# Kernel optimization log

Hardware: AMD Instinct MI355X
Metric: run time of the kernel (lower is better)

## Reference

```python
import jax, jax.numpy as jnp
import numpy as np

DYN = 16  # number of dynamic input features; x rows are [dynamic || static]


def setup_inputs() -> dict:
    key = jax.random.key(0)
    ks = jax.random.split(key, 20)
    T, S, H, O = 16384, 32, 512, 1
    sc_h = 1.0 / np.sqrt(H)
    inp = {
        "x": jax.random.normal(ks[0], (T, DYN + S), jnp.float32),
        "h0": jax.random.normal(ks[1], (H,), jnp.float32),
        "c0": jax.random.normal(ks[2], (H,), jnp.float32),
        "Wi": jax.random.normal(ks[3], (H, S), jnp.float32) / np.sqrt(S),
        "bi": jax.random.normal(ks[4], (H,), jnp.float32) * 0.1,
        "Wf1": jax.random.normal(ks[5], (H, DYN), jnp.float32) / np.sqrt(DYN),
        "bf1": jax.random.normal(ks[6], (H,), jnp.float32) * 0.1,
        "Wf2": jax.random.normal(ks[7], (H, H), jnp.float32) * sc_h,
        "bf2": jax.random.normal(ks[8], (H,), jnp.float32) * 0.1,
        "Wg1": jax.random.normal(ks[9], (H, DYN), jnp.float32) / np.sqrt(DYN),
        "bg1": jax.random.normal(ks[10], (H,), jnp.float32) * 0.1,
        "Wg2": jax.random.normal(ks[11], (H, H), jnp.float32) * sc_h,
        "bg2": jax.random.normal(ks[12], (H,), jnp.float32) * 0.1,
        "Wo1": jax.random.normal(ks[13], (H, DYN), jnp.float32) / np.sqrt(DYN),
        "bo1": jax.random.normal(ks[14], (H,), jnp.float32) * 0.1,
        "Wo2": jax.random.normal(ks[15], (H, H), jnp.float32) * sc_h,
        "bo2": jax.random.normal(ks[16], (H,), jnp.float32) * 0.1,
        "Wl": jax.random.normal(ks[17], (O, H), jnp.float32) * sc_h,
        "bl": jax.random.normal(ks[18], (O,), jnp.float32) * 0.1,
    }
    return inp


def reference(x, h0, c0, Wi, bi, Wf1, bf1, Wf2, bf2, Wg1, bg1, Wg2, bg2,
              Wo1, bo1, Wo2, bo2, Wl, bl):
    x_dyn = x[:, :DYN]   # [T, DYN]
    x_stat = x[:, DYN:]  # [T, S]
    # input gate depends only on static features -> vectorize over T
    i_all = jax.nn.sigmoid(x_stat @ Wi.T + bi)           # [T, H]
    # precompute dynamic-input projections (both linear biases folded in)
    pf = x_dyn @ Wf1.T + (bf1 + bf2)                      # [T, H]
    pg = x_dyn @ Wg1.T + (bg1 + bg2)
    po = x_dyn @ Wo1.T + (bo1 + bo2)

    def step(carry, ins):
        h, c = carry
        it, xf, xg, xo = ins
        f = jax.nn.sigmoid(xf + h @ Wf2.T)
        g = jnp.tanh(xg + h @ Wg2.T)
        o = jax.nn.sigmoid(xo + h @ Wo2.T)
        c = f * c + it * g
        h = o * jnp.tanh(c)
        return (h, c), h

    (_, _), h_all = jax.lax.scan(step, (h0, c0), (i_all, pf, pg, po))
    out = h_all @ Wl.T + bl                               # [T, O]
    return out
```

## Files before the change

kernel.cpp:

```cpp
#include <hip/hip_runtime.h>

#define T_STEPS 16384
#define HID     512
#define NSLOT   32
#define JPW     16
#define RING_D  8
#define RING_W  1024
#define NPART   (NSLOT * 4)
#define NBLK    256
#define FAST_TRIES 3

typedef unsigned u32x4 __attribute__((ext_vector_type(4)));

__device__ __forceinline__ unsigned ld_agent(const unsigned* p) {
  return __hip_atomic_load(p, __ATOMIC_RELAXED, __HIP_MEMORY_SCOPE_AGENT);
}
__device__ __forceinline__ float sigf(float x) {
  return __fdividef(1.f, 1.f + __expf(-x));
}
__device__ __forceinline__ float tanhfast(float x) {
  x = fminf(fmaxf(x, -15.f), 15.f);
  float e = __expf(2.f * x);
  return 1.f - __fdividef(2.f, e + 1.f);
}

__global__ void init_kernel(float* __restrict__ out,
                            unsigned* __restrict__ ring_fast,
                            unsigned* __restrict__ ring_slow,
                            const float* __restrict__ h0,
                            const float* __restrict__ bl) {
  int i = blockIdx.x * blockDim.x + threadIdx.x;
  if (i < T_STEPS) out[i] = bl[0];
  if (i < RING_D * RING_W) {
    unsigned v = 0;
    int slot = i >> 10;
    int w = i & (RING_W - 1);
    if (slot == RING_D - 1) {
      unsigned bits = __float_as_uint(h0[w >> 1]);
      v = (w & 1) ? ((bits << 16) | 1u) : ((bits & 0xFFFF0000u) | 1u);
    }
    ring_fast[i] = v;
    ring_slow[i] = v;
  }
}

__global__ void finalize_kernel(const float* __restrict__ part,
                                const float* __restrict__ bl,
                                float* __restrict__ out) {
  int t = blockIdx.x * blockDim.x + threadIdx.x;
  float s = bl[0];
#pragma unroll 8
  for (int i = 0; i < NPART; ++i) s += part[i * T_STEPS + t];
  out[t] = s;
}

__global__ __launch_bounds__(256, 1) void lstm_scan(
    const float* __restrict__ x,  const float* __restrict__ c0,
    const float* __restrict__ Wi, const float* __restrict__ bi,
    const float* __restrict__ Wf1,const float* __restrict__ bf1,
    const float* __restrict__ Wf2,const float* __restrict__ bf2,
    const float* __restrict__ Wg1,const float* __restrict__ bg1,
    const float* __restrict__ Wg2,const float* __restrict__ bg2,
    const float* __restrict__ Wo1,const float* __restrict__ bo1,
    const float* __restrict__ Wo2,const float* __restrict__ bo2,
    const float* __restrict__ Wl, float* __restrict__ out,
    unsigned* __restrict__ ring_fast, unsigned* __restrict__ ring_slow,
    float* __restrict__ part)
{
  if ((blockIdx.x & 7) != 0) return;
  const int slot = blockIdx.x >> 3;

  const int tid = threadIdx.x;
  const int jl  = tid >> 4;
  const int s   = tid & 15;
  const int jg  = slot * JPW + jl;

  __shared__ __align__(16) float hbuf[2][16 * 36];
  __shared__ float4 xbuf[2][12];

  float4 wf[8], wg[8], wo[8];
  {
    const float4* pf = (const float4*)(Wf2 + jg * HID + s * 32);
    const float4* pg = (const float4*)(Wg2 + jg * HID + s * 32);
    const float4* po = (const float4*)(Wo2 + jg * HID + s * 32);
#pragma unroll
    for (int r = 0; r < 8; ++r) { wf[r] = pf[r]; wg[r] = pg[r]; wo[r] = po[r]; }
  }
  float4 wx[8];
  float xb = 0.f;
#pragma unroll
  for (int r = 0; r < 8; ++r) wx[r] = make_float4(0.f, 0.f, 0.f, 0.f);
  if (s == 0) {
    const float4* p = (const float4*)(Wi + jg * 32);
#pragma unroll
    for (int r = 0; r < 8; ++r) wx[r] = p[r];
    xb = bi[jg];
  } else if (s == 1) {
    const float4* p = (const float4*)(Wf1 + jg * 16);
#pragma unroll
    for (int r = 0; r < 4; ++r) wx[r] = p[r];
    xb = bf1[jg] + bf2[jg];
  } else if (s == 2) {
    const float4* p = (const float4*)(Wg1 + jg * 16);
#pragma unroll
    for (int r = 0; r < 4; ++r) wx[r] = p[r];
    xb = bg1[jg] + bg2[jg];
  } else if (s == 3) {
    const float4* p = (const float4*)(Wo1 + jg * 16);
#pragma unroll
    for (int r = 0; r < 4; ++r) wx[r] = p[r];
    xb = bo1[jg] + bo2[jg];
  }

  float cst = c0[jg];
  const float wl = Wl[jg];

  float4 xpre = make_float4(0.f, 0.f, 0.f, 0.f);
  if (tid < 12) {
    xbuf[0][tid] = *(const float4*)(x + 4 * tid);
    xpre = *(const float4*)(x + 48 + 4 * tid);
  }
  __syncthreads();

  for (int t = 0; t < T_STEPS; ++t) {
    if (tid < 12) {
      xbuf[(t + 1) & 1][tid] = xpre;
      int tn = (t + 2 < T_STEPS) ? t + 2 : T_STEPS - 1;
      xpre = *(const float4*)(x + tn * 48 + 4 * tid);
    }
    float pr = xb;
    if (s < 4) {
      const float4* xv = &xbuf[t & 1][(s == 0) ? 4 : 0];
#pragma unroll
      for (int r = 0; r < 4; ++r) {
        float4 vv = xv[r], w = wx[r];
        pr = fmaf(w.x, vv.x, pr); pr = fmaf(w.y, vv.y, pr);
        pr = fmaf(w.z, vv.z, pr); pr = fmaf(w.w, vv.w, pr);
      }
      if (s == 0) {
#pragma unroll
        for (int r = 4; r < 8; ++r) {
          float4 vv = xv[r], w = wx[r];
          pr = fmaf(w.x, vv.x, pr); pr = fmaf(w.y, vv.y, pr);
          pr = fmaf(w.z, vv.z, pr); pr = fmaf(w.w, vv.w, pr);
        }
      }
    }
    float accf = (s == 1) ? pr : 0.f;
    float accg = (s == 2) ? pr : 0.f;
    float acco = (s == 3) ? pr : 0.f;
    const float ipre = pr;

    const unsigned want = (unsigned)(t + 1);
    const unsigned ring_off =
        (((unsigned)(t - 1)) & (RING_D - 1)) * RING_W + 4 * tid;
    unsigned a, b, c2, d2;
    unsigned matched = 0;
    {
      const unsigned* pf = ring_fast + ring_off;
#pragma unroll 1
      for (int k = 0; k < FAST_TRIES; ++k) {
        u32x4 v;
        asm volatile("global_load_dwordx4 %0, %1, off sc0\n\ts_waitcnt vmcnt(0)"
                     : "=v"(v) : "v"(pf) : "memory");
        a = v[0]; b = v[1]; c2 = v[2]; d2 = v[3];
        if (!(((a ^ want) | (b ^ want) | (c2 ^ want) | (d2 ^ want)) & 0xFFFFu)) {
          matched = 1;
          break;
        }
      }
    }
    if (!matched) {
      const unsigned* pw = ring_slow + ring_off;
      do {
        a = ld_agent(pw); b = ld_agent(pw + 1);
        c2 = ld_agent(pw + 2); d2 = ld_agent(pw + 3);
      } while (((a ^ want) | (b ^ want) | (c2 ^ want) | (d2 ^ want)) & 0xFFFFu);
    }
    unsigned bits0 = (a  & 0xFFFF0000u) | (b  >> 16);
    unsigned bits1 = (c2 & 0xFFFF0000u) | (d2 >> 16);
    {
      int idx = 2 * tid + 4 * (tid >> 4);
      *(float2*)(&hbuf[t & 1][idx]) =
          make_float2(__uint_as_float(bits0), __uint_as_float(bits1));
    }
    __syncthreads();

    const float* hb = &hbuf[t & 1][s * 36];
#pragma unroll
    for (int r = 0; r < 8; ++r) {
      float4 hv = *(const float4*)(hb + 4 * r);
      accf = fmaf(wf[r].x, hv.x, accf); accf = fmaf(wf[r].y, hv.y, accf);
      accf = fmaf(wf[r].z, hv.z, accf); accf = fmaf(wf[r].w, hv.w, accf);
      accg = fmaf(wg[r].x, hv.x, accg); accg = fmaf(wg[r].y, hv.y, accg);
      accg = fmaf(wg[r].z, hv.z, accg); accg = fmaf(wg[r].w, hv.w, accg);
      acco = fmaf(wo[r].x, hv.x, acco); acco = fmaf(wo[r].y, hv.y, acco);
      acco = fmaf(wo[r].z, hv.z, acco); acco = fmaf(wo[r].w, hv.w, acco);
    }
#pragma unroll
    for (int m = 1; m <= 8; m <<= 1) {
      accf += __shfl_xor(accf, m, 16);
      accg += __shfl_xor(accg, m, 16);
      acco += __shfl_xor(acco, m, 16);
    }
    float f  = sigf(accf);
    float g  = tanhfast(accg);
    float o  = sigf(acco);
    float it = sigf(ipre);
    cst = fmaf(f, cst, it * g);
    float hj = o * tanhfast(cst);

    if (s == 0) {
      unsigned bits = __float_as_uint(hj);
      unsigned tag  = (unsigned)(t + 2);
      unsigned long long v64 =
          (unsigned long long)((bits & 0xFFFF0000u) | tag) |
          ((unsigned long long)((bits << 16) | tag) << 32);
      unsigned dst_off = (t & (RING_D - 1)) * RING_W + 2 * jg;
      __hip_atomic_store((unsigned long long*)(ring_fast + dst_off), v64,
                         __ATOMIC_RELAXED, __HIP_MEMORY_SCOPE_WORKGROUP);
      __hip_atomic_store((unsigned long long*)(ring_slow + dst_off), v64,
                         __ATOMIC_RELAXED, __HIP_MEMORY_SCOPE_AGENT);
    }
    float val = (s == 0) ? wl * hj : 0.f;
    val += __shfl_xor(val, 16, 64);
    val += __shfl_xor(val, 32, 64);
    if ((tid & 63) == 0) {
      if (part) {
        part[(slot * 4 + (tid >> 6)) * T_STEPS + t] = val;
      } else {
        atomicAdd(out + t, val);
      }
    }
  }
}

extern "C" void kernel_launch(void* const* d_in, const int* in_sizes, int n_in,
                              void* d_out, int out_size, void* d_ws, size_t ws_size,
                              hipStream_t stream) {
  const float* x   = (const float*)d_in[0];
  const float* h0  = (const float*)d_in[1];
  const float* c0  = (const float*)d_in[2];
  const float* Wi  = (const float*)d_in[3];
  const float* bi  = (const float*)d_in[4];
  const float* Wf1 = (const float*)d_in[5];
  const float* bf1 = (const float*)d_in[6];
  const float* Wf2 = (const float*)d_in[7];
  const float* bf2 = (const float*)d_in[8];
  const float* Wg1 = (const float*)d_in[9];
  const float* bg1 = (const float*)d_in[10];
  const float* Wg2 = (const float*)d_in[11];
  const float* bg2 = (const float*)d_in[12];
  const float* Wo1 = (const float*)d_in[13];
  const float* bo1 = (const float*)d_in[14];
  const float* Wo2 = (const float*)d_in[15];
  const float* bo2 = (const float*)d_in[16];
  const float* Wl  = (const float*)d_in[17];
  const float* bl  = (const float*)d_in[18];
  float* out = (float*)d_out;

  size_t ring_words = (size_t)RING_D * RING_W;
  unsigned* ring_fast = (unsigned*)d_ws;
  unsigned* ring_slow = ring_fast + ring_words;
  size_t base_bytes = 2 * ring_words * 4;
  size_t part_bytes = (size_t)NPART * T_STEPS * 4;
  float* part = (ws_size >= base_bytes + part_bytes)
                    ? (float*)((char*)d_ws + base_bytes)
                    : nullptr;

  hipLaunchKernelGGL(init_kernel, dim3(64), dim3(256), 0, stream,
                     out, ring_fast, ring_slow, h0, bl);
  hipLaunchKernelGGL(lstm_scan, dim3(NBLK), dim3(256), 0, stream,
                     x, c0, Wi, bi, Wf1, bf1, Wf2, bf2, Wg1, bg1, Wg2, bg2,
                     Wo1, bo1, Wo2, bo2, Wl, out, ring_fast, ring_slow, part);
  if (part) {
    hipLaunchKernelGGL(finalize_kernel, dim3(T_STEPS / 256), dim3(256), 0, stream,
                       part, bl, out);
  }
}
```

Measured before the change: 30.98 ms.

## Unroll recurrence by 8, overlap ring poll with input projection, batch x staging

The time loop is unrolled in blocks of 8 steps. The first ring-buffer poll load is issued before the input-projection FMAs and waited on afterwards, so its latency is hidden behind useful work. Input rows are now staged 8 at a time into shared memory, and partial head outputs are written as float4 pairs once per block instead of once per step. The cross-lane shuffle reduction is replaced with DPP row adds, the barrier becomes a raw s_barrier with an explicit lgkmcnt wait, and the number of fast poll retries is raised. The cost is higher register pressure from the unroll and the pacc array.

```diff
diff --git a/kernel.cpp b/kernel.cpp
--- a/kernel.cpp
+++ b/kernel.cpp
@@ -8,7 +8,7 @@
 #define RING_W  1024
 #define NPART   (NSLOT * 4)
 #define NBLK    256
-#define FAST_TRIES 3
+#define FAST_TRIES 8
 
 typedef unsigned u32x4 __attribute__((ext_vector_type(4)));
 
@@ -22,6 +22,18 @@
   x = fminf(fmaxf(x, -15.f), 15.f);
   float e = __expf(2.f * x);
   return 1.f - __fdividef(2.f, e + 1.f);
+}
+template <int CTRL>
+__device__ __forceinline__ float dpp_xadd(float v) {
+  int t = __builtin_amdgcn_update_dpp(0, __float_as_int(v), CTRL, 0xF, 0xF, true);
+  return v + __int_as_float(t);
+}
+__device__ __forceinline__ float row16_reduce(float v) {
+  v = dpp_xadd<0xB1>(v);
+  v = dpp_xadd<0x4E>(v);
+  v = dpp_xadd<0x141>(v);
+  v = dpp_xadd<0x140>(v);
+  return v;
 }
 
 __global__ void init_kernel(float* __restrict__ out,
@@ -76,7 +88,7 @@
   const int jg  = slot * JPW + jl;
 
   __shared__ __align__(16) float hbuf[2][16 * 36];
-  __shared__ float4 xbuf[2][12];
+  __shared__ __align__(16) float4 xstage[2][96];
 
   float4 wf[8], wg[8], wo[8];
   {
@@ -115,121 +127,135 @@
   float cst = c0[jg];
   const float wl = Wl[jg];
 
+  const int xrow = tid / 12, xcol = tid - 12 * xrow;
   float4 xpre = make_float4(0.f, 0.f, 0.f, 0.f);
-  if (tid < 12) {
-    xbuf[0][tid] = *(const float4*)(x + 4 * tid);
-    xpre = *(const float4*)(x + 48 + 4 * tid);
+  if (tid < 96) {
+    xstage[0][tid] = *(const float4*)(x + xrow * 48 + 4 * xcol);
+    xpre = *(const float4*)(x + (8 + xrow) * 48 + 4 * xcol);
   }
   __syncthreads();
 
-  for (int t = 0; t < T_STEPS; ++t) {
-    if (tid < 12) {
-      xbuf[(t + 1) & 1][tid] = xpre;
-      int tn = (t + 2 < T_STEPS) ? t + 2 : T_STEPS - 1;
-      xpre = *(const float4*)(x + tn * 48 + 4 * tid);
-    }
-    float pr = xb;
-    if (s < 4) {
-      const float4* xv = &xbuf[t & 1][(s == 0) ? 4 : 0];
-#pragma unroll
-      for (int r = 0; r < 4; ++r) {
-        float4 vv = xv[r], w = wx[r];
-        pr = fmaf(w.x, vv.x, pr); pr = fmaf(w.y, vv.y, pr);
-        pr = fmaf(w.z, vv.z, pr); pr = fmaf(w.w, vv.w, pr);
-      }
-      if (s == 0) {
-#pragma unroll
-        for (int r = 4; r < 8; ++r) {
+  float pacc[8];
+
+  for (int tb = 0; tb < T_STEPS / 8; ++tb) {
+#pragma unroll
+    for (int u = 0; u < 8; ++u) {
+      const int t = tb * 8 + u;
+      const unsigned want = (unsigned)(t + 1);
+      const unsigned ring_off =
+          (((unsigned)(t - 1)) & (RING_D - 1)) * RING_W + 4 * tid;
+      const unsigned* pf = ring_fast + ring_off;
+      u32x4 v;
+      asm volatile("global_load_dwordx4 %0, %1, off sc0"
+                   : "=v"(v) : "v"(pf) : "memory");
+      float pr = xb;
+      if (s < 4) {
+        const float4* xv = &xstage[tb & 1][u * 12 + ((s == 0) ? 4 : 0)];
+#pragma unroll
+        for (int r = 0; r < 4; ++r) {
           float4 vv = xv[r], w = wx[r];
           pr = fmaf(w.x, vv.x, pr); pr = fmaf(w.y, vv.y, pr);
           pr = fmaf(w.z, vv.z, pr); pr = fmaf(w.w, vv.w, pr);
         }
-      }
+        if (s == 0) {
+#pragma unroll
+          for (int r = 4; r < 8; ++r) {
+            float4 vv = xv[r], w = wx[r];
+            pr = fmaf(w.x, vv.x, pr); pr = fmaf(w.y, vv.y, pr);
+            pr = fmaf(w.z, vv.z, pr); pr = fmaf(w.w, vv.w, pr);
+          }
+        }
+      }
+      float accf = (s == 1) ? pr : 0.f;
+      float accg = (s == 2) ? pr : 0.f;
+      float acco = (s == 3) ? pr : 0.f;
+      const float ipre = pr;
+
+      asm volatile("s_waitcnt vmcnt(0)" ::: "memory");
+      asm volatile("" : "+v"(v));
+      unsigned a = v[0], b = v[1], c2 = v[2], d2 = v[3];
+      if (((a ^ want) | (b ^ want) | (c2 ^ want) | (d2 ^ want)) & 0xFFFFu) {
+        unsigned matched = 0;
+#pragma unroll 1
+        for (int k = 1; k < FAST_TRIES; ++k) {
+          asm volatile("global_load_dwordx4 %0, %1, off sc0\n\ts_waitcnt vmcnt(0)"
+                       : "=v"(v) : "v"(pf) : "memory");
+          a = v[0]; b = v[1]; c2 = v[2]; d2 = v[3];
+          if (!(((a ^ want) | (b ^ want) | (c2 ^ want) | (d2 ^ want)) & 0xFFFFu)) {
+            matched = 1;
+            break;
+          }
+        }
+        if (!matched) {
+          const unsigned* pw = ring_slow + ring_off;
+          do {
+            a = ld_agent(pw); b = ld_agent(pw + 1);
+            c2 = ld_agent(pw + 2); d2 = ld_agent(pw + 3);
+          } while (((a ^ want) | (b ^ want) | (c2 ^ want) | (d2 ^ want)) & 0xFFFFu);
+        }
+      }
+      unsigned bits0 = (a  & 0xFFFF0000u) | (b  >> 16);
+      unsigned bits1 = (c2 & 0xFFFF0000u) | (d2 >> 16);
+      {
+        int idx = 2 * tid + 4 * (tid >> 4);
+        *(float2*)(&hbuf[t & 1][idx]) =
+            make_float2(__uint_as_float(bits0), __uint_as_float(bits1));
+      }
+      if (u == 7 && tid < 96) {
+        xstage[(tb + 1) & 1][tid] = xpre;
+        int row = (tb + 2) * 8 + xrow;
+        if (row >= T_STEPS) row = T_STEPS - 1;
+        xpre = *(const float4*)(x + row * 48 + 4 * xcol);
+      }
+      asm volatile("s_waitcnt lgkmcnt(0)" ::: "memory");
+      __builtin_amdgcn_s_barrier();
+
+      const float* hb = &hbuf[t & 1][s * 36];
+#pragma unroll
+      for (int r = 0; r < 8; ++r) {
+        float4 hv = *(const float4*)(hb + 4 * r);
+        accf = fmaf(wf[r].x, hv.x, accf); accf = fmaf(wf[r].y, hv.y, accf);
+        accf = fmaf(wf[r].z, hv.z, accf); accf = fmaf(wf[r].w, hv.w, accf);
+        accg = fmaf(wg[r].x, hv.x, accg); accg = fmaf(wg[r].y, hv.y, accg);
+        accg = fmaf(wg[r].z, hv.z, accg); accg = fmaf(wg[r].w, hv.w, accg);
+        acco = fmaf(wo[r].x, hv.x, acco); acco = fmaf(wo[r].y, hv.y, acco);
+        acco = fmaf(wo[r].z, hv.z, acco); acco = fmaf(wo[r].w, hv.w, acco);
+      }
+      accf = row16_reduce(accf);
+      accg = row16_reduce(accg);
+      acco = row16_reduce(acco);
+      float f  = sigf(accf);
+      float g  = tanhfast(accg);
+      float o  = sigf(acco);
+      float it = sigf(ipre);
+      cst = fmaf(f, cst, it * g);
+      float hj = o * tanhfast(cst);
+
+      if (s == 0) {
+        unsigned bits = __float_as_uint(hj);
+        unsigned tag  = (unsigned)(t + 2);
+        unsigned long long v64 =
+            (unsigned long long)((bits & 0xFFFF0000u) | tag) |
+            ((unsigned long long)((bits << 16) | tag) << 32);
+        unsigned dst_off = (t & (RING_D - 1)) * RING_W + 2 * jg;
+        __hip_atomic_store((unsigned long long*)(ring_fast + dst_off), v64,
+                           __ATOMIC_RELAXED, __HIP_MEMORY_SCOPE_WORKGROUP);
+        __hip_atomic_store((unsigned long long*)(ring_slow + dst_off), v64,
+                           __ATOMIC_RELAXED, __HIP_MEMORY_SCOPE_AGENT);
+      }
+      float val = (s == 0) ? wl * hj : 0.f;
+      val += __shfl_xor(val, 16, 64);
+      val += __shfl_xor(val, 32, 64);
+      pacc[u] = val;
     }
-    float accf = (s == 1) ? pr : 0.f;
-    float accg = (s == 2) ? pr : 0.f;
-    float acco = (s == 3) ? pr : 0.f;
-    const float ipre = pr;
-
-    const unsigned want = (unsigned)(t + 1);
-    const unsigned ring_off =
-        (((unsigned)(t - 1)) & (RING_D - 1)) * RING_W + 4 * tid;
-    unsigned a, b, c2, d2;
-    unsigned matched = 0;
-    {
-      const unsigned* pf = ring_fast + ring_off;
-#pragma unroll 1
-      for (int k = 0; k < FAST_TRIES; ++k) {
-        u32x4 v;
-        asm volatile("global_load_dwordx4 %0, %1, off sc0\n\ts_waitcnt vmcnt(0)"
-                     : "=v"(v) : "v"(pf) : "memory");
-        a = v[0]; b = v[1]; c2 = v[2]; d2 = v[3];
-        if (!(((a ^ want) | (b ^ want) | (c2 ^ want) | (d2 ^ want)) & 0xFFFFu)) {
-          matched = 1;
-          break;
-        }
-      }
-    }
-    if (!matched) {
-      const unsigned* pw = ring_slow + ring_off;
-      do {
-        a = ld_agent(pw); b = ld_agent(pw + 1);
-        c2 = ld_agent(pw + 2); d2 = ld_agent(pw + 3);
-      } while (((a ^ want) | (b ^ want) | (c2 ^ want) | (d2 ^ want)) & 0xFFFFu);
-    }
-    unsigned bits0 = (a  & 0xFFFF0000u) | (b  >> 16);
-    unsigned bits1 = (c2 & 0xFFFF0000u) | (d2 >> 16);
-    {
-      int idx = 2 * tid + 4 * (tid >> 4);
-      *(float2*)(&hbuf[t & 1][idx]) =
-          make_float2(__uint_as_float(bits0), __uint_as_float(bits1));
-    }
-    __syncthreads();
-
-    const float* hb = &hbuf[t & 1][s * 36];
-#pragma unroll
-    for (int r = 0; r < 8; ++r) {
-      float4 hv = *(const float4*)(hb + 4 * r);
-      accf = fmaf(wf[r].x, hv.x, accf); accf = fmaf(wf[r].y, hv.y, accf);
-      accf = fmaf(wf[r].z, hv.z, accf); accf = fmaf(wf[r].w, hv.w, accf);
-      accg = fmaf(wg[r].x, hv.x, accg); accg = fmaf(wg[r].y, hv.y, accg);
-      accg = fmaf(wg[r].z, hv.z, accg); accg = fmaf(wg[r].w, hv.w, accg);
-      acco = fmaf(wo[r].x, hv.x, acco); acco = fmaf(wo[r].y, hv.y, acco);
-      acco = fmaf(wo[r].z, hv.z, acco); acco = fmaf(wo[r].w, hv.w, acco);
-    }
-#pragma unroll
-    for (int m = 1; m <= 8; m <<= 1) {
-      accf += __shfl_xor(accf, m, 16);
-      accg += __shfl_xor(accg, m, 16);
-      acco += __shfl_xor(acco, m, 16);
-    }
-    float f  = sigf(accf);
-    float g  = tanhfast(accg);
-    float o  = sigf(acco);
-    float it = sigf(ipre);
-    cst = fmaf(f, cst, it * g);
-    float hj = o * tanhfast(cst);
-
-    if (s == 0) {
-      unsigned bits = __float_as_uint(hj);
-      unsigned tag  = (unsigned)(t + 2);
-      unsigned long long v64 =
-          (unsigned long long)((bits & 0xFFFF0000u) | tag) |
-          ((unsigned long long)((bits << 16) | tag) << 32);
-      unsigned dst_off = (t & (RING_D - 1)) * RING_W + 2 * jg;
-      __hip_atomic_store((unsigned long long*)(ring_fast + dst_off), v64,
-                         __ATOMIC_RELAXED, __HIP_MEMORY_SCOPE_WORKGROUP);
-      __hip_atomic_store((unsigned long long*)(ring_slow + dst_off), v64,
-                         __ATOMIC_RELAXED, __HIP_MEMORY_SCOPE_AGENT);
-    }
-    float val = (s == 0) ? wl * hj : 0.f;
-    val += __shfl_xor(val, 16, 64);
-    val += __shfl_xor(val, 32, 64);
     if ((tid & 63) == 0) {
       if (part) {
-        part[(slot * 4 + (tid >> 6)) * T_STEPS + t] = val;
+        float* dst = part + (slot * 4 + (tid >> 6)) * T_STEPS + tb * 8;
+        *(float4*)(dst)     = make_float4(pacc[0], pacc[1], pacc[2], pacc[3]);
+        *(float4*)(dst + 4) = make_float4(pacc[4], pacc[5], pacc[6], pacc[7]);
       } else {
-        atomicAdd(out + t, val);
+#pragma unroll
+        for (int u = 0; u < 8; ++u) atomicAdd(out + tb * 8 + u, pacc[u]);
       }
     }
   }
```

After: 28.83 ms. -6.9%, faster.
